# Performance work log

Measured on AMD Instinct MI355X. Metric: run time of the kernel, lower is better.

## Reference

```python
import jax, jax.numpy as jnp
import numpy as np

TEMP = 0.08
EPS = 1e-8
GAMMA = 0.99
BETA = 0.5 * (1.0 - GAMMA)  # alpha * (1 - gamma)
COS_EPS = 1e-8  # torch F.cosine_similarity norm-product clamp


def setup_inputs() -> dict:
    key = jax.random.key(0)
    k1, k2, k3 = jax.random.split(key, 3)
    B, D, C = 8192, 256, 7
    features = jax.random.normal(k1, (B, D), dtype=jnp.float32)
    labels = jax.random.randint(k2, (B,), 0, C)
    # orthogonal prototypes via QR, as in generate_orthogonal_vectors
    q, _ = jnp.linalg.qr(jax.random.normal(k3, (D, C), dtype=jnp.float32))
    prototypes = q.T  # [C, D]
    momentums = jnp.zeros((C, D), dtype=jnp.float32)
    return {"features": features, "labels": labels,
            "prototypes": prototypes, "momentums": momentums}


def _update_prototypes(features, labels, prototypes, momentums):
    # sequential EMA over the batch (repeated labels chain), as in the torch loop
    deltas = features - prototypes[labels]  # delta uses the OLD prototypes throughout

    def step(m, ld):
        l, d = ld
        return m.at[l].set(GAMMA * m[l] + BETA * d), None

    m_final, _ = jax.lax.scan(step, momentums, (labels, deltas))
    target = prototypes + m_final  # [C, D]
    q, _ = jnp.linalg.qr(target.T)  # reduced QR: [D, C]
    return q.T  # [C, D], re-orthogonalized prototypes


def reference(features, labels, prototypes, momentums):
    C = prototypes.shape[0]
    new_protos = _update_prototypes(features, labels, prototypes, momentums)

    feats = jnp.concatenate([features, new_protos], axis=0)          # [N, D]
    labs = jnp.concatenate([labels, jnp.arange(C, dtype=labels.dtype)])
    N = feats.shape[0]

    # cosine similarity matrix: dot / clamp(|x||y|, eps)  (matches F.cosine_similarity)
    nrm = jnp.linalg.norm(feats, axis=-1)                            # [N]
    sim = (feats @ feats.T) / jnp.maximum(nrm[:, None] * nrm[None, :], COS_EPS)
    scores = (1.0 + sim) * 0.5 + EPS

    offdiag = 1.0 - jnp.eye(N, dtype=scores.dtype)
    scores = scores * offdiag / TEMP
    scores = scores - jnp.max(scores)

    same = labs[:, None] == labs[None, :]                            # [N, N] bool
    pos_mask = same.astype(scores.dtype) * offdiag
    neg_mask = (~same).astype(scores.dtype)

    pos = jnp.sum(scores * pos_mask, axis=-1) / (jnp.sum(pos_mask, axis=-1) + EPS)
    neg = jnp.log(jnp.sum(jnp.exp(scores) * neg_mask, axis=-1) + EPS)
    loss = -pos + neg                                                # [N]

    m = loss > 0
    cnt = jnp.sum(m.astype(loss.dtype))
    mean_pos = jnp.sum(jnp.where(m, loss, 0.0)) / jnp.maximum(cnt, 1.0)
    return jnp.where(cnt > 0, mean_pos, jnp.array(0.0, loss.dtype))
```

## Files before the change

### kernel.cpp

```cpp
#include <hip/hip_runtime.h>
#include <stdint.h>

#define B    8192
#define D    256
#define C    7
#define NTOT 8199
#define NPAD 8320
#define NT   65
#define NBLK 2145
#define BETAC 0.005f
#define L2GAMMA (-0.0144995696951151f)
#define KC   (6.25f + 1.25e-7f)
#define EC1  9.016844005555771f
#define EC0  9.016844185925551f

using f32x4  = __attribute__((ext_vector_type(4))) float;

__device__ __forceinline__ void async16(const void* src, void* dst) {
    __builtin_amdgcn_global_load_lds(
        (const __attribute__((address_space(1))) void*)src,
        (__attribute__((address_space(3))) void*)dst, 16, 0, 0);
}

#define WAITVM(N) asm volatile("s_waitcnt vmcnt(" #N ")" ::: "memory")
#define BARRIER() do { __builtin_amdgcn_s_barrier(); asm volatile("" ::: "memory"); } while(0)

__global__ void kzero(float* __restrict__ z) {
    int t = threadIdx.x;
    for (int i = t; i < 1804; i += 256) z[i] = 0.f;
}

__global__ void kaccnorm(const float* __restrict__ feats, const int* __restrict__ labels,
                         float* __restrict__ S, unsigned* __restrict__ G32,
                         int* __restrict__ labs_ext, int* __restrict__ hist) {
    __shared__ int cnt[256 * 8];
    __shared__ int tot[8];
    __shared__ float wrow[32];
    __shared__ float sacc[4][7][256];
    int tid = threadIdx.x, lane = tid & 63, wv = tid >> 6;
    int bid = blockIdx.x;

    int lab[32];
    #pragma unroll
    for (int q = 0; q < 8; ++q) {
        int4 v = *(const int4*)(labels + tid * 32 + q * 4);
        lab[q * 4 + 0] = v.x; lab[q * 4 + 1] = v.y;
        lab[q * 4 + 2] = v.z; lab[q * 4 + 3] = v.w;
    }
    int myc[8] = {0, 0, 0, 0, 0, 0, 0, 0};
    #pragma unroll
    for (int k = 0; k < 32; ++k) {
        #pragma unroll
        for (int cc = 0; cc < 7; ++cc) myc[cc] += (lab[k] == cc) ? 1 : 0;
    }
    #pragma unroll
    for (int cc = 0; cc < 8; ++cc) cnt[tid * 8 + cc] = myc[cc];
    __syncthreads();
    for (int c = wv; c < C; c += 4) {
        int v[4], partial = 0;
        #pragma unroll
        for (int k = 0; k < 4; ++k) { v[k] = cnt[(lane * 4 + k) * 8 + c]; partial += v[k]; }
        int inc = partial;
        #pragma unroll
        for (int d = 1; d < 64; d <<= 1) {
            int y = __shfl_up(inc, d);
            if (lane >= d) inc += y;
        }
        int run = inc - partial;
        #pragma unroll
        for (int k = 0; k < 4; ++k) { int tmp = v[k]; cnt[(lane * 4 + k) * 8 + c] = run; run += tmp; }
        if (lane == 63) { tot[c] = inc; if (bid == 0) hist[c] = inc; }
    }
    __syncthreads();
    if (tid == 0) {
        int loc[7];
        #pragma unroll
        for (int cc = 0; cc < 7; ++cc) loc[cc] = cnt[bid * 8 + cc];
        for (int k = 0; k < 32; ++k) {
            int c2 = labels[bid * 32 + k];
            int r = ++loc[c2];
            wrow[k] = exp2f((float)(tot[c2] - r) * L2GAMMA);
        }
    }
    if (tid < 32) labs_ext[bid * 32 + tid] = labels[bid * 32 + tid];
    if (bid == 0) {
        if (tid < 128) { int i2 = B + tid; labs_ext[i2] = (i2 < NTOT) ? (i2 - B) : -1; }
        for (int i = tid; i < 121 * 64; i += 256) G32[NTOT * 64 + i] = 0u;
    }
    __syncthreads();

    float acc7[7][4] = {};
    int base = bid * 32 + wv * 8;
    for (int k = 0; k < 8; ++k) {
        int row = base + k;
        const float4 v = *(const float4*)(feats + (size_t)row * 256 + lane * 4);
        float ss = v.x * v.x + v.y * v.y + v.z * v.z + v.w * v.w;
        #pragma unroll
        for (int off = 1; off < 64; off <<= 1) ss += __shfl_xor(ss, off);
        float rn = 1.f / sqrtf(ss);
        unsigned p = (unsigned)__builtin_amdgcn_cvt_pk_fp8_f32(v.x * rn, v.y * rn, 0, false);
        p = (unsigned)__builtin_amdgcn_cvt_pk_fp8_f32(v.z * rn, v.w * rn, (int)p, true);
        G32[(size_t)row * 64 + lane] = p;
        int c = labels[row];
        float wgt = wrow[wv * 8 + k];
        #pragma unroll
        for (int cc = 0; cc < 7; ++cc)
            if (c == cc) {
                acc7[cc][0] += wgt * v.x; acc7[cc][1] += wgt * v.y;
                acc7[cc][2] += wgt * v.z; acc7[cc][3] += wgt * v.w;
            }
    }
    #pragma unroll
    for (int cc = 0; cc < 7; ++cc)
        #pragma unroll
        for (int jj = 0; jj < 4; ++jj) sacc[wv][cc][lane * 4 + jj] = acc7[cc][jj];
    __syncthreads();
    #pragma unroll
    for (int cc = 0; cc < 7; ++cc) {
        float s = sacc[0][cc][tid] + sacc[1][cc][tid] + sacc[2][cc][tid] + sacc[3][cc][tid];
        if (s != 0.f) atomicAdd(&S[cc * 256 + tid], s);
    }
}

__global__ __launch_bounds__(512, 2) void kmain(const unsigned char* __restrict__ G,
                                                unsigned* __restrict__ G32w,
                                                const int* __restrict__ labs,
                                                float* __restrict__ pP,
                                                float* __restrict__ pN,
                                                const float* __restrict__ S,
                                                const int* __restrict__ hist,
                                                const float* __restrict__ protos,
                                                const float* __restrict__ moms,
                                                unsigned* __restrict__ flag) {
    __shared__ unsigned char Asm_[128 * 256];
    __shared__ unsigned char Bsm_[128 * 256];
    __shared__ float vvs[8];
    __shared__ float bcast[8];
    float* rowP = (float*)Asm_;
    float* rowN = rowP + 256;
    float* colP = rowN + 256;
    float* colN = colP + 512;

    int b0 = blockIdx.x;
    int xcd = b0 & 7, pos = b0 >> 3;
    int b = (xcd == 0) ? pos : (269 + (xcd - 1) * 268 + pos);

    int jt = (int)((sqrtf(8.f * (float)b + 1.f) - 1.f) * 0.5f);
    while ((jt * (jt + 1)) / 2 > b) --jt;
    while (((jt + 1) * (jt + 2)) / 2 <= b) ++jt;
    int it = b - (jt * (jt + 1)) / 2;

    int rowA = it * 128, rowB = jt * 128;
    int tid = threadIdx.x, lane = tid & 63, w8 = tid >> 6;
    int wr = w8 >> 1, wc = w8 & 1;
    int g4 = lane >> 4, q15 = lane & 15;
    const char* gb = (const char*)G;

    if (b == 0) {
        float* Aq = (float*)Asm_;
        float* Vq = (float*)Bsm_;
        int t = tid, w = tid >> 6, ln = tid & 63;
        if (tid < 256) {
            #pragma unroll
            for (int c = 0; c < C; ++c) {
                float p = protos[c * 256 + t];
                float m0 = moms[c * 256 + t];
                float gn = exp2f((float)hist[c] * L2GAMMA);
                float mf = gn * m0 + BETAC * S[c * 256 + t] - 0.5f * (1.f - gn) * p;
                Aq[t * 8 + c] = p + mf;
                Vq[t * 8 + c] = 0.f;
            }
        }
        __syncthreads();
        for (int j = 0; j < C; ++j) {
            if (tid < 64) {
                float s = 0.f;
                for (int i = tid; i < 256; i += 64) {
                    float a = (i >= j) ? Aq[i * 8 + j] : 0.f;
                    s += a * a;
                }
                #pragma unroll
                for (int off = 32; off; off >>= 1) s += __shfl_xor(s, off);
                if (tid == 0) {
                    float norm = sqrtf(s);
                    float alpha = Aq[j * 8 + j];
                    float beta = (alpha >= 0.f) ? -norm : norm;
                    float vv = 2.f * beta * (beta - alpha);
                    bcast[0] = alpha; bcast[1] = beta;
                    bcast[2] = (vv > 0.f) ? 1.f : 0.f;
                    vvs[j] = (vv > 0.f) ? vv : 1.f;
                }
            }
            __syncthreads();
            if (tid < 256) {
                float alpha = bcast[0], valid = bcast[2];
                float beta = bcast[1];
                float vi = 0.f;
                if (valid != 0.f) {
                    if (t == j) vi = alpha - beta;
                    else if (t > j) vi = Aq[t * 8 + j];
                }
                Vq[t * 8 + j] = vi;
            }
            __syncthreads();
            if (tid < 256) {
                float vvj = vvs[j];
                for (int k = j + 1 + w; k < C; k += 4) {
                    float cp = 0.f;
                    for (int i = ln; i < 256; i += 64) cp += Vq[i * 8 + j] * Aq[i * 8 + k];
                    #pragma unroll
                    for (int off = 32; off; off >>= 1) cp += __shfl_xor(cp, off);
                    float scale = 2.f * cp / vvj;
                    for (int i = ln; i < 256; i += 64) Aq[i * 8 + k] -= scale * Vq[i * 8 + j];
                }
            }
            __syncthreads();
        }
        if (tid < 256) {
            #pragma unroll
            for (int c = 0; c < C; ++c) Aq[t * 8 + c] = (t == c) ? 1.f : 0.f;
        }
        __syncthreads();
        for (int j = C - 1; j >= 0; --j) {
            if (tid < 256) {
                float vvj = vvs[j];
                for (int k = w; k < C; k += 4) {
                    float cp = 0.f;
                    for (int i = ln; i < 256; i += 64) cp += Vq[i * 8 + j] * Aq[i * 8 + k];
                    #pragma unroll
                    for (int off = 32; off; off >>= 1) cp += __shfl_xor(cp, off);
                    float scale = 2.f * cp / vvj;
                    for (int i = ln; i < 256; i += 64) Aq[i * 8 + k] -= scale * Vq[i * 8 + j];
                }
            }
            __syncthreads();
        }
        if (tid < 256) {
            for (int c = w; c < C; c += 4) {
                float s = 0.f;
                for (int i = ln; i < 256; i += 64) { float a = Aq[i * 8 + c]; s += a * a; }
                #pragma unroll
                for (int off = 32; off; off >>= 1) s += __shfl_xor(s, off);
                if (ln == 0) bcast[c] = 1.f / sqrtf(s);
            }
        }
        __syncthreads();
        if (tid < 256) {
            unsigned char* G8 = (unsigned char*)G32w;
            #pragma unroll
            for (int c = 0; c < C; ++c) {
                float val = Aq[t * 8 + c] * bcast[c];
                int pk = __builtin_amdgcn_cvt_pk_fp8_f32(val, 0.f, 0, false);
                G8[(size_t)(B + c) * 256 + t] = (unsigned char)(pk & 0xff);
            }
        }
        __syncthreads();
        if (tid == 0) { __threadfence(); atomicExch(flag, 1u); }
    }

    bool protoTile = (jt == NT - 1);
    if (protoTile) {
        if (tid == 0) {
            while (atomicAdd(flag, 0u) == 0u) __builtin_amdgcn_s_sleep(32);
        }
        __syncthreads();
    }

    #pragma unroll
    for (int q = 0; q < 4; ++q) {
        int o = q * 8192 + tid * 16;
        int row = o >> 8, colb = o & 255;
        int sc = colb ^ ((row & 15) << 4);
        async16(gb + (size_t)(rowA + row) * 256 + sc, (char*)Asm_ + o);
    }
    #pragma unroll
    for (int q = 0; q < 4; ++q) {
        int o = q * 8192 + tid * 16;
        int row = o >> 8, colb = o & 255;
        int sc = colb ^ ((row & 15) << 4);
        async16(gb + (size_t)(rowB + row) * 256 + sc, (char*)Bsm_ + o);
    }

    int ljv[4];
    #pragma unroll
    for (int n = 0; n < 4; ++n) ljv[n] = labs[rowB + wc * 64 + n * 16 + q15];
    int4 lrow[2];
    #pragma unroll
    for (int m = 0; m < 2; ++m)
        lrow[m] = *(const int4*)(labs + rowA + wr * 32 + m * 16 + g4 * 4);

    f32x4 acc[2][4];
    #pragma unroll
    for (int m = 0; m < 2; ++m)
        #pragma unroll
        for (int n = 0; n < 4; ++n) acc[m][n] = 0.f;

    WAITVM(0);
    BARRIER();

    if (protoTile) {
        if (tid < 448) {
            int c = tid >> 6, l = tid & 63;
            unsigned v = atomicAdd(&G32w[(size_t)(B + c) * 64 + l], 0u);
            int off = c * 256 + ((((l >> 2) ^ c) << 4) | ((l & 3) << 2));
            *(unsigned*)((char*)Bsm_ + off) = v;
            if (it == NT - 1) *(unsigned*)((char*)Asm_ + off) = v;
        }
        __syncthreads();
    }

    #pragma unroll
    for (int kk = 0; kk < 8; ++kk) {
        long af[2], bfr[4];
        int cb = (kk * 32 + g4 * 8) ^ (q15 << 4);
        #pragma unroll
        for (int m = 0; m < 2; ++m) {
            int r0 = wr * 32 + m * 16 + q15;
            af[m] = *(const long*)((const char*)Asm_ + r0 * 256 + cb);
        }
        #pragma unroll
        for (int n = 0; n < 4; ++n) {
            int r0 = wc * 64 + n * 16 + q15;
            bfr[n] = *(const long*)((const char*)Bsm_ + r0 * 256 + cb);
        }
        __builtin_amdgcn_s_setprio(1);
        #pragma unroll
        for (int m = 0; m < 2; ++m)
            #pragma unroll
            for (int n = 0; n < 4; ++n)
                acc[m][n] = __builtin_amdgcn_mfma_f32_16x16x32_fp8_fp8(af[m], bfr[n], acc[m][n], 0, 0, 0);
        __builtin_amdgcn_s_setprio(0);
    }

    __syncthreads();

    float cs[4] = {0.f, 0.f, 0.f, 0.f}, cn[4] = {0.f, 0.f, 0.f, 0.f};
    bool fastpath = (it != jt) && (jt != NT - 1);

#define EPI(VALIDEXPR)                                                         \
    _Pragma("unroll")                                                          \
    for (int m = 0; m < 2; ++m) {                                              \
        _Pragma("unroll")                                                      \
        for (int r = 0; r < 4; ++r) {                                          \
            int il = wr * 32 + m * 16 + g4 * 4 + r;                            \
            int i = rowA + il; (void)i;                                        \
            int li = ((const int*)&lrow[m])[r];                                \
            float ps = 0.f, ns = 0.f;                                          \
            _Pragma("unroll")                                                  \
            for (int n = 0; n < 4; ++n) {                                      \
                int j = rowB + wc * 64 + n * 16 + q15; (void)j;                \
                float sim = acc[m][n][r];                                      \
                float s = fmaf(sim, 6.25f, KC);                                \
                float e = exp2f(fmaf(sim, EC1, EC0));                          \
                if (VALIDEXPR) {                                               \
                    if (li == ljv[n]) { ps += s; cs[n] += s; }                 \
                    else              { ns += e; cn[n] += e; }                 \
                }                                                              \
            }                                                                  \
            _Pragma("unroll")                                                  \
            for (int off = 1; off < 16; off <<= 1) {                           \
                ps += __shfl_xor(ps, off);                                     \
                ns += __shfl_xor(ns, off);                                     \
            }                                                                  \
            if (q15 == 0) { rowP[wc * 128 + il] = ps; rowN[wc * 128 + il] = ns; } \
        }                                                                      \
    }

    if (fastpath) { EPI(true); }
    else          { EPI(i < NTOT && j < NTOT && i != j); }
#undef EPI

    #pragma unroll
    for (int n = 0; n < 4; ++n) {
        float a = cs[n], bb = cn[n];
        a += __shfl_xor(a, 16); a += __shfl_xor(a, 32);
        bb += __shfl_xor(bb, 16); bb += __shfl_xor(bb, 32);
        if (g4 == 0) {
            colP[wr * 128 + wc * 64 + n * 16 + q15] = a;
            colN[wr * 128 + wc * 64 + n * 16 + q15] = bb;
        }
    }

    __syncthreads();
    if (tid < 128) {
        pP[(size_t)jt * NPAD + rowA + tid] = rowP[tid] + rowP[128 + tid];
        pN[(size_t)jt * NPAD + rowA + tid] = rowN[tid] + rowN[128 + tid];
    } else if (tid < 256 && it != jt) {
        int tt = tid - 128;
        pP[(size_t)it * NPAD + rowB + tt] = colP[tt] + colP[128 + tt] + colP[256 + tt] + colP[384 + tt];
        pN[(size_t)it * NPAD + rowB + tt] = colN[tt] + colN[128 + tt] + colN[256 + tt] + colN[384 + tt];
    }
}

__global__ void kreduce(const float* __restrict__ pP, const float* __restrict__ pN,
                        const int* __restrict__ hist, const int* __restrict__ labs,
                        float* __restrict__ lossacc, unsigned* __restrict__ ticket,
                        float* __restrict__ out) {
    int i = blockIdx.x * 256 + threadIdx.x;
    float lsum = 0.f, lcnt = 0.f;
    if (i < NTOT) {
        float sp = 0.f, sn = 0.f;
        #pragma unroll 5
        for (int c = 0; c < NT; ++c) {
            sp += pP[(size_t)c * NPAD + i];
            sn += pN[(size_t)c * NPAD + i];
        }
        float cnt = (float)hist[labs[i]];
        float pos = sp / (cnt + 1e-8f);
        float neg = logf(sn + 1e-8f);
        float loss = neg - pos;
        if (loss > 0.f) { lsum = loss; lcnt = 1.f; }
    }
    #pragma unroll
    for (int off = 1; off < 64; off <<= 1) {
        lsum += __shfl_xor(lsum, off);
        lcnt += __shfl_xor(lcnt, off);
    }
    __shared__ float s1[4], s2[4];
    int lane = threadIdx.x & 63, w = threadIdx.x >> 6;
    if (lane == 0) { s1[w] = lsum; s2[w] = lcnt; }
    __syncthreads();
    if (threadIdx.x == 0) {
        atomicAdd(&lossacc[0], s1[0] + s1[1] + s1[2] + s1[3]);
        atomicAdd(&lossacc[1], s2[0] + s2[1] + s2[2] + s2[3]);
        __threadfence();
        unsigned tk = atomicAdd(ticket, 1u);
        if (tk == 32) {
            float a = atomicAdd(&lossacc[0], 0.f);
            float c2 = atomicAdd(&lossacc[1], 0.f);
            out[0] = (c2 > 0.f) ? a / fmaxf(c2, 1.f) : 0.f;
        }
    }
}

extern "C" void kernel_launch(void* const* d_in, const int* in_sizes, int n_in,
                              void* d_out, int out_size, void* d_ws, size_t ws_size,
                              hipStream_t stream) {
    const float* feats  = (const float*)d_in[0];
    const int*   labels = (const int*)d_in[1];
    const float* protos = (const float*)d_in[2];
    const float* moms   = (const float*)d_in[3];
    float* out = (float*)d_out;

    char* ws = (char*)d_ws;
    float*    S_      = (float*)(ws + 0);
    int*      hist    = (int*)  (ws + 7168);
    float*    lossacc = (float*)(ws + 7200);
    unsigned* ticket  = (unsigned*)(ws + 7208);
    unsigned* flag    = (unsigned*)(ws + 7212);
    int*      labs    = (int*)  (ws + 7296);
    unsigned char* G  = (unsigned char*)(ws + 40704);
    float*    pP      = (float*)(ws + 2170624);
    float*    pN      = (float*)(ws + 4333824);

    kzero<<<1, 256, 0, stream>>>((float*)ws);
    kaccnorm<<<256, 256, 0, stream>>>(feats, labels, S_, (unsigned*)G, labs, hist);
    kmain<<<NBLK, 512, 0, stream>>>(G, (unsigned*)G, labs, pP, pN, S_, hist,
                                    protos, moms, flag);
    kreduce<<<33, 256, 0, stream>>>(pP, pN, hist, labs, lossacc, ticket, out);
}
```

Measured before the change: 87.90 us.

## Split tile load into two K-halves and overlap second half with first MFMAs

The 128x256 fp8 tiles are now loaded as two K-halves stored in separate 128-byte-row LDS regions with a new XOR swizzle. The kernel waits only on the first half (vmcnt 4), runs four MFMA k-steps on it, then waits for the second half. This is meant to hide part of the global-to-LDS load latency behind compute. The prototype row atomic read is also issued before the tile loads, and its LDS write is split across the two halves. It adds an extra barrier and changes the swizzle, which risks bank conflicts or layout mistakes.

```diff
diff --git a/kernel.cpp b/kernel.cpp
--- a/kernel.cpp
+++ b/kernel.cpp
@@ -24,6 +24,7 @@
 
 #define WAITVM(N) asm volatile("s_waitcnt vmcnt(" #N ")" ::: "memory")
 #define BARRIER() do { __builtin_amdgcn_s_barrier(); asm volatile("" ::: "memory"); } while(0)
+#define CFENCE() asm volatile("" ::: "memory")
 
 __global__ void kzero(float* __restrict__ z) {
     int t = threadIdx.x;
@@ -132,8 +133,8 @@
                                                 const float* __restrict__ protos,
                                                 const float* __restrict__ moms,
                                                 unsigned* __restrict__ flag) {
-    __shared__ unsigned char Asm_[128 * 256];
-    __shared__ unsigned char Bsm_[128 * 256];
+    __shared__ unsigned char Asm_[32768];
+    __shared__ unsigned char Bsm_[32768];
     __shared__ float vvs[8];
     __shared__ float bcast[8];
     float* rowP = (float*)Asm_;
@@ -259,26 +260,17 @@
     }
 
     bool protoTile = (jt == NT - 1);
+    unsigned pv = 0; int pc = 0, pl = 0, poff = 0;
     if (protoTile) {
         if (tid == 0) {
             while (atomicAdd(flag, 0u) == 0u) __builtin_amdgcn_s_sleep(32);
         }
         __syncthreads();
-    }
-
-    #pragma unroll
-    for (int q = 0; q < 4; ++q) {
-        int o = q * 8192 + tid * 16;
-        int row = o >> 8, colb = o & 255;
-        int sc = colb ^ ((row & 15) << 4);
-        async16(gb + (size_t)(rowA + row) * 256 + sc, (char*)Asm_ + o);
-    }
-    #pragma unroll
-    for (int q = 0; q < 4; ++q) {
-        int o = q * 8192 + tid * 16;
-        int row = o >> 8, colb = o & 255;
-        int sc = colb ^ ((row & 15) << 4);
-        async16(gb + (size_t)(rowB + row) * 256 + sc, (char*)Bsm_ + o);
+        if (tid < 448) {
+            pc = tid >> 6; pl = tid & 63;
+            pv = atomicAdd(&G32w[(size_t)(B + pc) * 64 + pl], 0u);
+            poff = ((pl >= 32) ? 16384 : 0) + pc * 128 + (((pl & 31) << 2) ^ ((pc & 7) << 4));
+        }
     }
 
     int ljv[4];
@@ -288,40 +280,88 @@
     #pragma unroll
     for (int m = 0; m < 2; ++m)
         lrow[m] = *(const int4*)(labs + rowA + wr * 32 + m * 16 + g4 * 4);
+    CFENCE();
+
+    #pragma unroll
+    for (int q = 0; q < 2; ++q) {
+        int o = q * 8192 + tid * 16;
+        int row = o >> 7, colb = o & 127;
+        int sc = colb ^ ((row & 7) << 4);
+        async16(gb + (size_t)(rowA + row) * 256 + 0 + sc, (char*)Asm_ + o);
+        async16(gb + (size_t)(rowB + row) * 256 + 0 + sc, (char*)Bsm_ + o);
+    }
+    CFENCE();
+    #pragma unroll
+    for (int q = 0; q < 2; ++q) {
+        int o = q * 8192 + tid * 16;
+        int row = o >> 7, colb = o & 127;
+        int sc = colb ^ ((row & 7) << 4);
+        async16(gb + (size_t)(rowA + row) * 256 + 128 + sc, (char*)Asm_ + 16384 + o);
+        async16(gb + (size_t)(rowB + row) * 256 + 128 + sc, (char*)Bsm_ + 16384 + o);
+    }
 
     f32x4 acc[2][4];
     #pragma unroll
     for (int m = 0; m < 2; ++m)
         #pragma unroll
         for (int n = 0; n < 4; ++n) acc[m][n] = 0.f;
+
+    WAITVM(4);
+    BARRIER();
+    if (protoTile) {
+        if (tid < 448 && pl < 32) {
+            *(unsigned*)((char*)Bsm_ + poff) = pv;
+            if (it == NT - 1) *(unsigned*)((char*)Asm_ + poff) = pv;
+        }
+        __syncthreads();
+    }
+
+    #pragma unroll
+    for (int kk = 0; kk < 4; ++kk) {
+        long af[2], bfr[4];
+        int cb = (kk * 32 + g4 * 8) ^ ((q15 & 7) << 4);
+        #pragma unroll
+        for (int m = 0; m < 2; ++m) {
+            int r0 = wr * 32 + m * 16 + q15;
+            af[m] = *(const long*)((const char*)Asm_ + r0 * 128 + cb);
+        }
+        #pragma unroll
+        for (int n = 0; n < 4; ++n) {
+            int r0 = wc * 64 + n * 16 + q15;
+            bfr[n] = *(const long*)((const char*)Bsm_ + r0 * 128 + cb);
+        }
+        __builtin_amdgcn_s_setprio(1);
+        #pragma unroll
+        for (int m = 0; m < 2; ++m)
+            #pragma unroll
+            for (int n = 0; n < 4; ++n)
+                acc[m][n] = __builtin_amdgcn_mfma_f32_16x16x32_fp8_fp8(af[m], bfr[n], acc[m][n], 0, 0, 0);
+        __builtin_amdgcn_s_setprio(0);
+    }
 
     WAITVM(0);
     BARRIER();
-
     if (protoTile) {
-        if (tid < 448) {
-            int c = tid >> 6, l = tid & 63;
-            unsigned v = atomicAdd(&G32w[(size_t)(B + c) * 64 + l], 0u);
-            int off = c * 256 + ((((l >> 2) ^ c) << 4) | ((l & 3) << 2));
-            *(unsigned*)((char*)Bsm_ + off) = v;
-            if (it == NT - 1) *(unsigned*)((char*)Asm_ + off) = v;
-        }
-        __syncthreads();
-    }
-
-    #pragma unroll
-    for (int kk = 0; kk < 8; ++kk) {
+        if (tid < 448 && pl >= 32) {
+            *(unsigned*)((char*)Bsm_ + poff) = pv;
+            if (it == NT - 1) *(unsigned*)((char*)Asm_ + poff) = pv;
+        }
+        __syncthreads();
+    }
+
+    #pragma unroll
+    for (int kk = 0; kk < 4; ++kk) {
         long af[2], bfr[4];
-        int cb = (kk * 32 + g4 * 8) ^ (q15 << 4);
+        int cb = (kk * 32 + g4 * 8) ^ ((q15 & 7) << 4);
         #pragma unroll
         for (int m = 0; m < 2; ++m) {
             int r0 = wr * 32 + m * 16 + q15;
-            af[m] = *(const long*)((const char*)Asm_ + r0 * 256 + cb);
+            af[m] = *(const long*)((const char*)Asm_ + 16384 + r0 * 128 + cb);
         }
         #pragma unroll
         for (int n = 0; n < 4; ++n) {
             int r0 = wc * 64 + n * 16 + q15;
-            bfr[n] = *(const long*)((const char*)Bsm_ + r0 * 256 + cb);
+            bfr[n] = *(const long*)((const char*)Bsm_ + 16384 + r0 * 128 + cb);
         }
         __builtin_amdgcn_s_setprio(1);
         #pragma unroll
```

Measured after the change: 87.73 us. About the same (-0.2%).

## Move prototype QR into last kaccnorm block via ticket, drop spin-wait in kmain

Applied to the files above, without the earlier changes.

The Householder QR of the updated prototypes moves out of kmain block 0 into whichever kaccnorm block finishes last, chosen with an atomic ticket counter. kmain no longer has a serial QR block, a flag spin-wait for the prototype tiles, or atomic reloads of the prototype rows into shared memory. This takes a serial, latency-bound step and the inter-block dependency off kmain's critical path. The cost is that one kaccnorm block now runs the QR serially at the tail of that kernel. It also depends on tot[] holding the global label counts in every block.

```diff
diff --git a/kernel.cpp b/kernel.cpp
--- a/kernel.cpp
+++ b/kernel.cpp
@@ -32,11 +32,16 @@
 
 __global__ void kaccnorm(const float* __restrict__ feats, const int* __restrict__ labels,
                          float* __restrict__ S, unsigned* __restrict__ G32,
-                         int* __restrict__ labs_ext, int* __restrict__ hist) {
+                         int* __restrict__ labs_ext, int* __restrict__ hist,
+                         const float* __restrict__ protos, const float* __restrict__ moms,
+                         unsigned* __restrict__ ticket2) {
     __shared__ int cnt[256 * 8];
     __shared__ int tot[8];
     __shared__ float wrow[32];
     __shared__ float sacc[4][7][256];
+    __shared__ float vvs[8];
+    __shared__ float bcast[8];
+    __shared__ int flagL;
     int tid = threadIdx.x, lane = tid & 63, wv = tid >> 6;
     int bid = blockIdx.x;
 
@@ -120,22 +125,104 @@
         float s = sacc[0][cc][tid] + sacc[1][cc][tid] + sacc[2][cc][tid] + sacc[3][cc][tid];
         if (s != 0.f) atomicAdd(&S[cc * 256 + tid], s);
     }
+    __syncthreads();
+    if (tid == 0) { __threadfence(); flagL = (int)atomicAdd(ticket2, 1u); }
+    __syncthreads();
+    if (flagL != 255) return;
+
+    int t = tid, w = wv, ln = lane;
+    float* Aq = &sacc[0][0][0];
+    float* Vq = Aq + 2048;
+    __syncthreads();
+    #pragma unroll
+    for (int c = 0; c < C; ++c) {
+        float p = protos[c * 256 + t];
+        float m0 = moms[c * 256 + t];
+        float gn = exp2f((float)tot[c] * L2GAMMA);
+        float sv = atomicAdd(&S[c * 256 + t], 0.f);
+        float mf = gn * m0 + BETAC * sv - 0.5f * (1.f - gn) * p;
+        Aq[t * 8 + c] = p + mf;
+        Vq[t * 8 + c] = 0.f;
+    }
+    __syncthreads();
+    for (int j = 0; j < C; ++j) {
+        if (w == 0) {
+            float s = 0.f;
+            for (int i = ln; i < 256; i += 64) {
+                float a = (i >= j) ? Aq[i * 8 + j] : 0.f;
+                s += a * a;
+            }
+            #pragma unroll
+            for (int off = 32; off; off >>= 1) s += __shfl_xor(s, off);
+            if (ln == 0) {
+                float norm = sqrtf(s);
+                float alpha = Aq[j * 8 + j];
+                float beta = (alpha >= 0.f) ? -norm : norm;
+                float vv = 2.f * beta * (beta - alpha);
+                bcast[0] = alpha; bcast[1] = beta;
+                bcast[2] = (vv > 0.f) ? 1.f : 0.f;
+                vvs[j] = (vv > 0.f) ? vv : 1.f;
+            }
+        }
+        __syncthreads();
+        float alpha = bcast[0], valid = bcast[2];
+        float beta = bcast[1];
+        float vi = 0.f;
+        if (valid != 0.f) {
+            if (t == j) vi = alpha - beta;
+            else if (t > j) vi = Aq[t * 8 + j];
+        }
+        Vq[t * 8 + j] = vi;
+        __syncthreads();
+        float vvj = vvs[j];
+        for (int k = j + 1 + w; k < C; k += 4) {
+            float cp = 0.f;
+            for (int i = ln; i < 256; i += 64) cp += Vq[i * 8 + j] * Aq[i * 8 + k];
+            #pragma unroll
+            for (int off = 32; off; off >>= 1) cp += __shfl_xor(cp, off);
+            float scale = 2.f * cp / vvj;
+            for (int i = ln; i < 256; i += 64) Aq[i * 8 + k] -= scale * Vq[i * 8 + j];
+        }
+        __syncthreads();
+    }
+    #pragma unroll
+    for (int c = 0; c < C; ++c) Aq[t * 8 + c] = (t == c) ? 1.f : 0.f;
+    __syncthreads();
+    for (int j = C - 1; j >= 0; --j) {
+        float vvj = vvs[j];
+        for (int k = w; k < C; k += 4) {
+            float cp = 0.f;
+            for (int i = ln; i < 256; i += 64) cp += Vq[i * 8 + j] * Aq[i * 8 + k];
+            #pragma unroll
+            for (int off = 32; off; off >>= 1) cp += __shfl_xor(cp, off);
+            float scale = 2.f * cp / vvj;
+            for (int i = ln; i < 256; i += 64) Aq[i * 8 + k] -= scale * Vq[i * 8 + j];
+        }
+        __syncthreads();
+    }
+    for (int c = w; c < C; c += 4) {
+        float s = 0.f;
+        for (int i = ln; i < 256; i += 64) { float a = Aq[i * 8 + c]; s += a * a; }
+        #pragma unroll
+        for (int off = 32; off; off >>= 1) s += __shfl_xor(s, off);
+        if (ln == 0) bcast[c] = 1.f / sqrtf(s);
+    }
+    __syncthreads();
+    unsigned char* G8 = (unsigned char*)G32;
+    #pragma unroll
+    for (int c = 0; c < C; ++c) {
+        float val = Aq[t * 8 + c] * bcast[c];
+        int pk = __builtin_amdgcn_cvt_pk_fp8_f32(val, 0.f, 0, false);
+        G8[(size_t)(B + c) * 256 + t] = (unsigned char)(pk & 0xff);
+    }
 }
 
 __global__ __launch_bounds__(512, 2) void kmain(const unsigned char* __restrict__ G,
-                                                unsigned* __restrict__ G32w,
                                                 const int* __restrict__ labs,
                                                 float* __restrict__ pP,
-                                                float* __restrict__ pN,
-                                                const float* __restrict__ S,
-                                                const int* __restrict__ hist,
-                                                const float* __restrict__ protos,
-                                                const float* __restrict__ moms,
-                                                unsigned* __restrict__ flag) {
+                                                float* __restrict__ pN) {
     __shared__ unsigned char Asm_[128 * 256];
     __shared__ unsigned char Bsm_[128 * 256];
-    __shared__ float vvs[8];
-    __shared__ float bcast[8];
     float* rowP = (float*)Asm_;
     float* rowN = rowP + 256;
     float* colP = rowN + 256;
@@ -156,116 +243,6 @@
     int g4 = lane >> 4, q15 = lane & 15;
     const char* gb = (const char*)G;
 
-    if (b == 0) {
-        float* Aq = (float*)Asm_;
-        float* Vq = (float*)Bsm_;
-        int t = tid, w = tid >> 6, ln = tid & 63;
-        if (tid < 256) {
-            #pragma unroll
-            for (int c = 0; c < C; ++c) {
-                float p = protos[c * 256 + t];
-                float m0 = moms[c * 256 + t];
-                float gn = exp2f((float)hist[c] * L2GAMMA);
-                float mf = gn * m0 + BETAC * S[c * 256 + t] - 0.5f * (1.f - gn) * p;
-                Aq[t * 8 + c] = p + mf;
-                Vq[t * 8 + c] = 0.f;
-            }
-        }
-        __syncthreads();
-        for (int j = 0; j < C; ++j) {
-            if (tid < 64) {
-                float s = 0.f;
-                for (int i = tid; i < 256; i += 64) {
-                    float a = (i >= j) ? Aq[i * 8 + j] : 0.f;
-                    s += a * a;
-                }
-                #pragma unroll
-                for (int off = 32; off; off >>= 1) s += __shfl_xor(s, off);
-                if (tid == 0) {
-                    float norm = sqrtf(s);
-                    float alpha = Aq[j * 8 + j];
-                    float beta = (alpha >= 0.f) ? -norm : norm;
-                    float vv = 2.f * beta * (beta - alpha);
-                    bcast[0] = alpha; bcast[1] = beta;
-                    bcast[2] = (vv > 0.f) ? 1.f : 0.f;
-                    vvs[j] = (vv > 0.f) ? vv : 1.f;
-                }
-            }
-            __syncthreads();
-            if (tid < 256) {
-                float alpha = bcast[0], valid = bcast[2];
-                float beta = bcast[1];
-                float vi = 0.f;
-                if (valid != 0.f) {
-                    if (t == j) vi = alpha - beta;
-                    else if (t > j) vi = Aq[t * 8 + j];
-                }
-                Vq[t * 8 + j] = vi;
-            }
-            __syncthreads();
-            if (tid < 256) {
-                float vvj = vvs[j];
-                for (int k = j + 1 + w; k < C; k += 4) {
-                    float cp = 0.f;
-                    for (int i = ln; i < 256; i += 64) cp += Vq[i * 8 + j] * Aq[i * 8 + k];
-                    #pragma unroll
-                    for (int off = 32; off; off >>= 1) cp += __shfl_xor(cp, off);
-                    float scale = 2.f * cp / vvj;
-                    for (int i = ln; i < 256; i += 64) Aq[i * 8 + k] -= scale * Vq[i * 8 + j];
-                }
-            }
-            __syncthreads();
-        }
-        if (tid < 256) {
-            #pragma unroll
-            for (int c = 0; c < C; ++c) Aq[t * 8 + c] = (t == c) ? 1.f : 0.f;
-        }
-        __syncthreads();
-        for (int j = C - 1; j >= 0; --j) {
-            if (tid < 256) {
-                float vvj = vvs[j];
-                for (int k = w; k < C; k += 4) {
-                    float cp = 0.f;
-                    for (int i = ln; i < 256; i += 64) cp += Vq[i * 8 + j] * Aq[i * 8 + k];
-                    #pragma unroll
-                    for (int off = 32; off; off >>= 1) cp += __shfl_xor(cp, off);
-                    float scale = 2.f * cp / vvj;
-                    for (int i = ln; i < 256; i += 64) Aq[i * 8 + k] -= scale * Vq[i * 8 + j];
-                }
-            }
-            __syncthreads();
-        }
-        if (tid < 256) {
-            for (int c = w; c < C; c += 4) {
-                float s = 0.f;
-                for (int i = ln; i < 256; i += 64) { float a = Aq[i * 8 + c]; s += a * a; }
-                #pragma unroll
-                for (int off = 32; off; off >>= 1) s += __shfl_xor(s, off);
-                if (ln == 0) bcast[c] = 1.f / sqrtf(s);
-            }
-        }
-        __syncthreads();
-        if (tid < 256) {
-            unsigned char* G8 = (unsigned char*)G32w;
-            #pragma unroll
-            for (int c = 0; c < C; ++c) {
-                float val = Aq[t * 8 + c] * bcast[c];
-                int pk = __builtin_amdgcn_cvt_pk_fp8_f32(val, 0.f, 0, false);
-                G8[(size_t)(B + c) * 256 + t] = (unsigned char)(pk & 0xff);
-            }
-        }
-        __syncthreads();
-        if (tid == 0) { __threadfence(); atomicExch(flag, 1u); }
-    }
-
-    bool protoTile = (jt == NT - 1);
-    if (protoTile) {
-        if (tid == 0) {
-            while (atomicAdd(flag, 0u) == 0u) __builtin_amdgcn_s_sleep(32);
-        }
-        __syncthreads();
-    }
-
     #pragma unroll
     for (int q = 0; q < 4; ++q) {
         int o = q * 8192 + tid * 16;
@@ -297,17 +274,6 @@
 
     WAITVM(0);
     BARRIER();
-
-    if (protoTile) {
-        if (tid < 448) {
-            int c = tid >> 6, l = tid & 63;
-            unsigned v = atomicAdd(&G32w[(size_t)(B + c) * 64 + l], 0u);
-            int off = c * 256 + ((((l >> 2) ^ c) << 4) | ((l & 3) << 2));
-            *(unsigned*)((char*)Bsm_ + off) = v;
-            if (it == NT - 1) *(unsigned*)((char*)Asm_ + off) = v;
-        }
-        __syncthreads();
-    }
 
     #pragma unroll
     for (int kk = 0; kk < 8; ++kk) {
@@ -447,15 +413,15 @@
     int*      hist    = (int*)  (ws + 7168);
     float*    lossacc = (float*)(ws + 7200);
     unsigned* ticket  = (unsigned*)(ws + 7208);
-    unsigned* flag    = (unsigned*)(ws + 7212);
+    unsigned* ticket2 = (unsigned*)(ws + 7212);
     int*      labs    = (int*)  (ws + 7296);
     unsigned char* G  = (unsigned char*)(ws + 40704);
     float*    pP      = (float*)(ws + 2170624);
     float*    pN      = (float*)(ws + 4333824);
 
     kzero<<<1, 256, 0, stream>>>((float*)ws);
-    kaccnorm<<<256, 256, 0, stream>>>(feats, labels, S_, (unsigned*)G, labs, hist);
-    kmain<<<NBLK, 512, 0, stream>>>(G, (unsigned*)G, labs, pP, pN, S_, hist,
-                                    protos, moms, flag);
+    kaccnorm<<<256, 256, 0, stream>>>(feats, labels, S_, (unsigned*)G, labs, hist,
+                                      protos, moms, ticket2);
+    kmain<<<NBLK, 512, 0, stream>>>(G, labs, pP, pN);
     kreduce<<<33, 256, 0, stream>>>(pP, pN, hist, labs, lossacc, ticket, out);
 }
```

New measurement: 107.8 us. 1.23x slower.
